# Kernel optimization log

Hardware: AMD Instinct MI355X
Metric: run time of the kernel (lower is better)

## Reference

```python
import jax, jax.numpy as jnp
import numpy as np
from jax import lax

B, D_IN, H, D_OUT, DEPTH = 16384, 1024, 1024, 256, 7


def setup_inputs() -> dict:
    key = jax.random.key(0)
    ks = jax.random.split(key, 10)
    f = jax.random.normal
    return {
        "x": f(ks[0], (B, D_IN), dtype=jnp.float32),
        "w0": f(ks[1], (D_IN, H), dtype=jnp.float32),
        "b0": f(ks[2], (H,), dtype=jnp.float32),
        "w1": f(ks[3], (H, H), dtype=jnp.float32),
        "b1": f(ks[4], (H,), dtype=jnp.float32),
        "tw": f(ks[5], (DEPTH, H, H), dtype=jnp.float32),   # transcendent_weights
        "cw": f(ks[6], (H, H), dtype=jnp.float32),           # classical_weights
        "cb": f(ks[7], (H,), dtype=jnp.float32),             # classical_biases (+ transcendent_biases folded out; original never uses transcendent_biases in forward)
        "wout": f(ks[8], (H, D_OUT), dtype=jnp.float32),
        "bout": f(ks[9], (D_OUT,), dtype=jnp.float32),
    }


def _transcendent_probs(tw):
    # tw: (DEPTH, n, m); angles used are tw[depth, j, 0:3] for j in range(out_dim)
    D, n, _ = tw.shape
    out_dim = n  # square layer: output_dimensions == input_dimensions
    angles = tw[:, :out_dim, :3]  # (D, O, 3)
    # each 'gate' matrix is the circulant M[i,i]=cos, M[i,i+1]=-sin, M[i+1,i]=sin (indices mod n)
    # => (M s)[i] = cos*s[i] - sin*s[i+1] + sin*s[i-1]  (circular shifts)
    state0 = jnp.full((out_dim, n), 1.0 / np.sqrt(n), dtype=tw.dtype)

    def gate(st, ang):  # st: (O, n), ang: (O,)
        c = jnp.cos(ang)[:, None]
        s = jnp.sin(ang)[:, None]
        return c * st - s * jnp.roll(st, -1, axis=1) + s * jnp.roll(st, 1, axis=1)

    def depth_step(st, a3):  # a3: (O, 3) -> consciousness, intelligence, wisdom gates
        st = gate(st, a3[:, 0])
        st = gate(st, a3[:, 1])
        st = gate(st, a3[:, 2])
        return st, None

    state, _ = lax.scan(depth_step, state0, angles)
    return jnp.abs(state[:, 0]) ** 2  # (O,), identical for every batch row


def reference(x, w0, b0, w1, b1, tw, cw, cb, wout, bout):
    h = jax.nn.relu(x @ w0 + b0)
    h = jax.nn.relu(h @ w1 + b1)
    # TranscendentNeuralLayer: tanh(classical + transcendent)
    h = jnp.tanh(h @ cw + cb + _transcendent_probs(tw)[None, :])
    return jax.nn.relu(h @ wout + bout)
```

## Files before the change

### kernel.cpp

```cpp
#include <hip/hip_runtime.h>
#include <hip/hip_bf16.h>

typedef __attribute__((ext_vector_type(8))) short bf16x8;
typedef __attribute__((ext_vector_type(4))) float f32x4;
typedef unsigned short u16;

__device__ __forceinline__ u16 f2bf(float f) {
  union { float f; unsigned int u; } v; v.f = f;
  unsigned int r = v.u + 0x7fffu + ((v.u >> 16) & 1u);
  return (u16)(r >> 16);
}
__device__ __forceinline__ float bf2f(u16 h) {
  union { unsigned int u; float f; } v; v.u = ((unsigned int)h) << 16;
  return v.f;
}

__device__ __forceinline__ void gload16(const void* g, void* l) {
  __builtin_amdgcn_global_load_lds(
      (const __attribute__((address_space(1))) unsigned int*)g,
      (__attribute__((address_space(3))) unsigned int*)l, 16, 0, 0);
}

__global__ void probs_kernel(const float* __restrict__ tw, float* __restrict__ probs) {
  int i = blockIdx.x * blockDim.x + threadIdx.x;
  if (i >= 1024) return;
  float p = 1.f;
  for (int d = 0; d < 7; ++d) {
    const float* a = tw + ((size_t)d * 1024 + i) * 1024;
    p *= cosf(a[0]) * cosf(a[1]) * cosf(a[2]);
  }
  probs[i] = p * p * (1.0f / 1024.0f);
}

__global__ void transpose_split(const float* __restrict__ src, u16* __restrict__ dhi,
                                u16* __restrict__ dlo, int R, int C) {
  __shared__ float t[32][33];
  int c0 = blockIdx.x * 32, r0 = blockIdx.y * 32;
  int tx = threadIdx.x, ty = threadIdx.y;
  #pragma unroll
  for (int p = 0; p < 4; ++p)
    t[ty + p * 8][tx] = src[(size_t)(r0 + ty + p * 8) * C + c0 + tx];
  __syncthreads();
  #pragma unroll
  for (int p = 0; p < 4; ++p) {
    float v = t[tx][ty + p * 8];
    u16 hi = f2bf(v);
    u16 lo = f2bf(v - bf2f(hi));
    size_t idx = (size_t)(c0 + ty + p * 8) * R + r0 + tx;
    dhi[idx] = hi; dlo[idx] = lo;
  }
}

__global__ void split_elem(const float* __restrict__ src, u16* __restrict__ hi,
                           u16* __restrict__ lo, int n4) {
  int i = blockIdx.x * blockDim.x + threadIdx.x;
  if (i >= n4) return;
  float4 v = ((const float4*)src)[i];
  ushort4 h, l;
  h.x = f2bf(v.x); l.x = f2bf(v.x - bf2f(h.x));
  h.y = f2bf(v.y); l.y = f2bf(v.y - bf2f(h.y));
  h.z = f2bf(v.z); l.z = f2bf(v.z - bf2f(h.z));
  h.w = f2bf(v.w); l.w = f2bf(v.w - bf2f(h.w));
  ((ushort4*)hi)[i] = h; ((ushort4*)lo)[i] = l;
}

template <int EPI>
__global__ __launch_bounds__(512, 2) void gemm256(
    const u16* __restrict__ Ahi, const u16* __restrict__ Alo,
    const u16* __restrict__ Bhi, const u16* __restrict__ Blo,
    const float* __restrict__ bias, const float* __restrict__ extra,
    u16* __restrict__ Ohi, u16* __restrict__ Olo,
    int N, int K, int nbx) {
  extern __shared__ __align__(16) char smem[];
  const int tid = threadIdx.x;
  const int wave = tid >> 6, lane = tid & 63;

  const int bq = gridDim.x >> 3;
  const int wg = (blockIdx.x & 7) * bq + (blockIdx.x >> 3);
  const int m0 = (wg / nbx) * 256, n0 = (wg % nbx) * 256;

  const int wm = (wave >> 2) * 128;
  const int wn = (wave & 3) * 64;
  const int lr = lane & 15, s0 = lane >> 4;

  f32x4 acc[8][4] = {};
  const int NT = K >> 5;

  auto stage = [&](const u16* __restrict__ G, int gr0, int kt, int ubase) {
    #pragma unroll
    for (int p = 0; p < 2; ++p) {
      const int ch = p * 8 + wave;
      const int off = ch * 1024 + lane * 16;
      const int r = off >> 6;
      const int s = ((off >> 4) & 3) ^ ((r >> 1) & 3);
      const u16* src = G + (size_t)(gr0 + r) * K + kt * 32 + s * 8;
      gload16((const void*)src, (void*)(smem + ubase + ch * 1024));
    }
  };
  auto frag = [&](int ubase, int row) -> bf16x8 {
    const int byte = ubase + row * 64 + ((s0 ^ ((row >> 1) & 3)) << 4);
    return *(const bf16x8*)(smem + byte);
  };

  stage(Ahi, m0, 0, 0);
  stage(Bhi, n0, 0, 32768);
  stage(Blo, n0, 0, 49152);
  stage(Alo, m0, 0, 16384);
  asm volatile("s_waitcnt vmcnt(4)" ::: "memory");
  __builtin_amdgcn_s_barrier();

  for (int kt = 0; kt < NT; ++kt) {
    const int cb = (kt & 1) << 16;
    const int nb = cb ^ 65536;
    const int kn = (kt + 1 == NT) ? 0 : kt + 1;
    bf16x8 a[8], bh[4], bl[4];

    stage(Ahi, m0, kn, nb);
    stage(Bhi, n0, kn, nb + 32768);
    #pragma unroll
    for (int m = 0; m < 8; ++m) a[m] = frag(cb, wm + m * 16 + lr);
    #pragma unroll
    for (int n = 0; n < 4; ++n) bh[n] = frag(cb + 32768, wn + n * 16 + lr);
    asm volatile("" ::: "memory");
    __builtin_amdgcn_s_barrier();
    __builtin_amdgcn_s_setprio(1);
    #pragma unroll
    for (int m = 0; m < 8; ++m)
      #pragma unroll
      for (int n = 0; n < 4; ++n)
        acc[m][n] = __builtin_amdgcn_mfma_f32_16x16x32_bf16(a[m], bh[n], acc[m][n], 0, 0, 0);
    __builtin_amdgcn_s_setprio(0);
    asm volatile("s_waitcnt vmcnt(6)" ::: "memory");
    __builtin_amdgcn_s_barrier();

    stage(Blo, n0, kn, nb + 49152);
    #pragma unroll
    for (int n = 0; n < 4; ++n) bl[n] = frag(cb + 49152, wn + n * 16 + lr);
    asm volatile("" ::: "memory");
    __builtin_amdgcn_s_barrier();
    __builtin_amdgcn_s_setprio(1);
    #pragma unroll
    for (int m = 0; m < 8; ++m)
      #pragma unroll
      for (int n = 0; n < 4; ++n)
        acc[m][n] = __builtin_amdgcn_mfma_f32_16x16x32_bf16(a[m], bl[n], acc[m][n], 0, 0, 0);
    __builtin_amdgcn_s_setprio(0);
    asm volatile("s_waitcnt vmcnt(6)" ::: "memory");
    __builtin_amdgcn_s_barrier();

    stage(Alo, m0, kn, nb + 16384);
    #pragma unroll
    for (int m = 0; m < 8; ++m) a[m] = frag(cb + 16384, wm + m * 16 + lr);
    asm volatile("" ::: "memory");
    __builtin_amdgcn_s_barrier();
    __builtin_amdgcn_s_setprio(1);
    #pragma unroll
    for (int m = 0; m < 8; ++m)
      #pragma unroll
      for (int n = 0; n < 4; ++n)
        acc[m][n] = __builtin_amdgcn_mfma_f32_16x16x32_bf16(a[m], bh[n], acc[m][n], 0, 0, 0);
    __builtin_amdgcn_s_setprio(0);
    asm volatile("s_waitcnt vmcnt(4)" ::: "memory");
    __builtin_amdgcn_s_barrier();
  }

  const int lm = lane >> 4, ln = lane & 15;
  float bsum[4];
  #pragma unroll
  for (int n = 0; n < 4; ++n) {
    int col = n0 + wn + n * 16 + ln;
    bsum[n] = bias[col];
    if (EPI == 1) bsum[n] += extra[col];
  }
  #pragma unroll
  for (int m = 0; m < 8; ++m) {
    int rbase = m0 + wm + m * 16 + lm * 4;
    #pragma unroll
    for (int n = 0; n < 4; ++n) {
      int col = n0 + wn + n * 16 + ln;
      #pragma unroll
      for (int r = 0; r < 4; ++r) {
        float v = acc[m][n][r] + bsum[n];
        if (EPI == 0) v = fmaxf(v, 0.f);
        else          v = 1.f - __fdividef(2.f, __expf(2.f * v) + 1.f);
        size_t idx = (size_t)(rbase + r) * N + col;
        u16 hi = f2bf(v);
        u16 lo = f2bf(v - bf2f(hi));
        Ohi[idx] = hi; Olo[idx] = lo;
      }
    }
  }
}

template <int EPI>
__global__ __launch_bounds__(256, 2) void gemm3(
    const u16* __restrict__ Ahi, const u16* __restrict__ Alo,
    const u16* __restrict__ Bhi, const u16* __restrict__ Blo,
    const float* __restrict__ bias, float* __restrict__ Ofp,
    int M, int N, int K) {
  __shared__ __align__(16) u16 sA[2][128 * 32];
  __shared__ __align__(16) u16 sB[2][128 * 32];

  const int tid = threadIdx.x;
  const int wave = tid >> 6;
  const int lane = tid & 63;
  const int n0 = blockIdx.x * 128;
  const int m0 = blockIdx.y * 128;
  const int wm = (wave >> 1) * 64;
  const int wn = (wave & 1) * 64;

  f32x4 acc[4][4] = {};

  const u16* gA[2] = {Ahi, Alo};
  const u16* gB[2] = {Bhi, Blo};
  const int srow = (lane >> 2);
  const int sslot = (lane & 3) * 8;

  for (int kt = 0; kt < K; kt += 32) {
    #pragma unroll
    for (int h = 0; h < 2; ++h) {
      #pragma unroll
      for (int j = 0; j < 2; ++j) {
        int c = wave * 2 + j;
        const u16* srcA = gA[h] + (size_t)(m0 + c * 16 + srow) * K + kt + sslot;
        gload16((const void*)srcA, (void*)&sA[h][c * 512]);
        const u16* srcB = gB[h] + (size_t)(n0 + c * 16 + srow) * K + kt + sslot;
        gload16((const void*)srcB, (void*)&sB[h][c * 512]);
      }
    }
    __syncthreads();

    const int kb = (lane >> 4) * 8;
    bf16x8 bh[4], bl[4];
    #pragma unroll
    for (int n = 0; n < 4; ++n) {
      int col = wn + n * 16 + (lane & 15);
      bh[n] = *(const bf16x8*)&sB[0][col * 32 + kb];
      bl[n] = *(const bf16x8*)&sB[1][col * 32 + kb];
    }
    #pragma unroll
    for (int m = 0; m < 4; ++m) {
      int row = wm + m * 16 + (lane & 15);
      bf16x8 ah = *(const bf16x8*)&sA[0][row * 32 + kb];
      bf16x8 al = *(const bf16x8*)&sA[1][row * 32 + kb];
      #pragma unroll
      for (int n = 0; n < 4; ++n) {
        acc[m][n] = __builtin_amdgcn_mfma_f32_16x16x32_bf16(ah, bh[n], acc[m][n], 0, 0, 0);
        acc[m][n] = __builtin_amdgcn_mfma_f32_16x16x32_bf16(ah, bl[n], acc[m][n], 0, 0, 0);
        acc[m][n] = __builtin_amdgcn_mfma_f32_16x16x32_bf16(al, bh[n], acc[m][n], 0, 0, 0);
      }
    }
    __syncthreads();
  }

  const int lm = lane >> 4;
  const int ln = lane & 15;
  float bsum[4];
  #pragma unroll
  for (int n = 0; n < 4; ++n) bsum[n] = bias[n0 + wn + n * 16 + ln];
  #pragma unroll
  for (int m = 0; m < 4; ++m) {
    int rbase = m0 + wm + m * 16 + lm * 4;
    #pragma unroll
    for (int n = 0; n < 4; ++n) {
      int col = n0 + wn + n * 16 + ln;
      #pragma unroll
      for (int r = 0; r < 4; ++r) {
        float v = acc[m][n][r] + bsum[n];
        Ofp[(size_t)(rbase + r) * N + col] = fmaxf(v, 0.f);
      }
    }
  }
}

extern "C" void kernel_launch(void* const* d_in, const int* in_sizes, int n_in,
                              void* d_out, int out_size, void* d_ws, size_t ws_size,
                              hipStream_t stream) {
  const float* x    = (const float*)d_in[0];
  const float* w0   = (const float*)d_in[1];
  const float* b0   = (const float*)d_in[2];
  const float* w1   = (const float*)d_in[3];
  const float* b1   = (const float*)d_in[4];
  const float* tw   = (const float*)d_in[5];
  const float* cw   = (const float*)d_in[6];
  const float* cb   = (const float*)d_in[7];
  const float* wout = (const float*)d_in[8];
  const float* bout = (const float*)d_in[9];
  float* out = (float*)d_out;
  char* ws = (char*)d_ws;
  const size_t MB = 1ull << 20;

  float* probs  = (float*)ws;
  u16* w0Thi = (u16*)(ws + 1 * MB);
  u16* w0Tlo = (u16*)(ws + 3 * MB);
  u16* w1Thi = (u16*)(ws + 5 * MB);
  u16* w1Tlo = (u16*)(ws + 7 * MB);
  u16* cwThi = (u16*)(ws + 9 * MB);
  u16* cwTlo = (u16*)(ws + 11 * MB);
  u16* woThi = (u16*)(ws + 13 * MB);
  u16* woTlo = (u16*)(ws + 13 * MB + 512 * 1024);
  u16* r0hi = (u16*)(ws + 16 * MB);
  u16* r0lo = (u16*)(ws + 48 * MB);
  u16* r1hi = (u16*)(ws + 80 * MB);
  u16* r1lo = (u16*)(ws + 112 * MB);

  hipFuncSetAttribute(reinterpret_cast<const void*>(gemm256<0>),
                      hipFuncAttributeMaxDynamicSharedMemorySize, 131072);
  hipFuncSetAttribute(reinterpret_cast<const void*>(gemm256<1>),
                      hipFuncAttributeMaxDynamicSharedMemorySize, 131072);

  probs_kernel<<<4, 256, 0, stream>>>(tw, probs);
  dim3 tb(32, 8);
  transpose_split<<<dim3(32, 32), tb, 0, stream>>>(w0, w0Thi, w0Tlo, 1024, 1024);
  transpose_split<<<dim3(32, 32), tb, 0, stream>>>(w1, w1Thi, w1Tlo, 1024, 1024);
  transpose_split<<<dim3(32, 32), tb, 0, stream>>>(cw, cwThi, cwTlo, 1024, 1024);
  transpose_split<<<dim3(8, 32), tb, 0, stream>>>(wout, woThi, woTlo, 1024, 256);
  split_elem<<<16384, 256, 0, stream>>>(x, r0hi, r0lo, 16384 * 1024 / 4);

  gemm256<0><<<256, 512, 131072, stream>>>(r0hi, r0lo, w0Thi, w0Tlo, b0, nullptr,
                                           r1hi, r1lo, 1024, 1024, 4);
  gemm256<0><<<256, 512, 131072, stream>>>(r1hi, r1lo, w1Thi, w1Tlo, b1, nullptr,
                                           r0hi, r0lo, 1024, 1024, 4);
  gemm256<1><<<256, 512, 131072, stream>>>(r0hi, r0lo, cwThi, cwTlo, cb, probs,
                                           r1hi, r1lo, 1024, 1024, 4);
  gemm3<2><<<dim3(2, 128), 256, 0, stream>>>(r1hi, r1lo, woThi, woTlo, bout,
                                             out, 16384, 256, 1024);
}
```

Baseline: 448.7 us.

## Switch big GEMMs to 32x32 MFMA, merge prep kernels, split-K bf16 last layer

New measurement: 447.4 us. Within noise of the previous version (-0.3%).

```diff
diff --git a/kernel.cpp b/kernel.cpp
--- a/kernel.cpp
+++ b/kernel.cpp
@@ -3,6 +3,7 @@
 
 typedef __attribute__((ext_vector_type(8))) short bf16x8;
 typedef __attribute__((ext_vector_type(4))) float f32x4;
+typedef __attribute__((ext_vector_type(16))) float f32x16;
 typedef unsigned short u16;
 
 __device__ __forceinline__ u16 f2bf(float f) {
@@ -21,22 +22,12 @@
       (__attribute__((address_space(3))) unsigned int*)l, 16, 0, 0);
 }
 
-__global__ void probs_kernel(const float* __restrict__ tw, float* __restrict__ probs) {
-  int i = blockIdx.x * blockDim.x + threadIdx.x;
-  if (i >= 1024) return;
-  float p = 1.f;
-  for (int d = 0; d < 7; ++d) {
-    const float* a = tw + ((size_t)d * 1024 + i) * 1024;
-    p *= cosf(a[0]) * cosf(a[1]) * cosf(a[2]);
-  }
-  probs[i] = p * p * (1.0f / 1024.0f);
-}
-
-__global__ void transpose_split(const float* __restrict__ src, u16* __restrict__ dhi,
-                                u16* __restrict__ dlo, int R, int C) {
+__device__ __forceinline__ void do_transpose(const float* __restrict__ src,
+                                             u16* __restrict__ dhi, u16* __restrict__ dlo,
+                                             int R, int C, int bx, int by, int tid) {
   __shared__ float t[32][33];
-  int c0 = blockIdx.x * 32, r0 = blockIdx.y * 32;
-  int tx = threadIdx.x, ty = threadIdx.y;
+  int c0 = bx * 32, r0 = by * 32;
+  int tx = tid & 31, ty = tid >> 5;
   #pragma unroll
   for (int p = 0; p < 4; ++p)
     t[ty + p * 8][tx] = src[(size_t)(r0 + ty + p * 8) * C + c0 + tx];
@@ -51,17 +42,41 @@
   }
 }
 
-__global__ void split_elem(const float* __restrict__ src, u16* __restrict__ hi,
-                           u16* __restrict__ lo, int n4) {
-  int i = blockIdx.x * blockDim.x + threadIdx.x;
-  if (i >= n4) return;
-  float4 v = ((const float4*)src)[i];
-  ushort4 h, l;
-  h.x = f2bf(v.x); l.x = f2bf(v.x - bf2f(h.x));
-  h.y = f2bf(v.y); l.y = f2bf(v.y - bf2f(h.y));
-  h.z = f2bf(v.z); l.z = f2bf(v.z - bf2f(h.z));
-  h.w = f2bf(v.w); l.w = f2bf(v.w - bf2f(h.w));
-  ((ushort4*)hi)[i] = h; ((ushort4*)lo)[i] = l;
+__global__ void prep_kernel(const float* __restrict__ tw, float* __restrict__ probs,
+                            const float* __restrict__ w0, u16* w0hi, u16* w0lo,
+                            const float* __restrict__ w1, u16* w1hi, u16* w1lo,
+                            const float* __restrict__ cw, u16* cwhi, u16* cwlo,
+                            const float* __restrict__ wo, u16* wohi, u16* wolo,
+                            const float* __restrict__ x, u16* xhi, u16* xlo) {
+  const int b = blockIdx.x, tid = threadIdx.x;
+  if (b < 4) {
+    int i = b * 256 + tid;
+    float p = 1.f;
+    for (int d = 0; d < 7; ++d) {
+      const float* a = tw + ((size_t)d * 1024 + i) * 1024;
+      p *= cosf(a[0]) * cosf(a[1]) * cosf(a[2]);
+    }
+    probs[i] = p * p * (1.0f / 1024.0f);
+  } else if (b < 1028) {
+    int bb = b - 4;    do_transpose(w0, w0hi, w0lo, 1024, 1024, bb & 31, bb >> 5, tid);
+  } else if (b < 2052) {
+    int bb = b - 1028; do_transpose(w1, w1hi, w1lo, 1024, 1024, bb & 31, bb >> 5, tid);
+  } else if (b < 3076) {
+    int bb = b - 2052; do_transpose(cw, cwhi, cwlo, 1024, 1024, bb & 31, bb >> 5, tid);
+  } else if (b < 3332) {
+    int bb = b - 3076; do_transpose(wo, wohi, wolo, 1024, 256, bb & 7, bb >> 3, tid);
+  } else {
+    int i = (b - 3332) * 256 + tid;
+    if (i < 16384 * 1024 / 4) {
+      float4 v = ((const float4*)x)[i];
+      ushort4 h, l;
+      h.x = f2bf(v.x); l.x = f2bf(v.x - bf2f(h.x));
+      h.y = f2bf(v.y); l.y = f2bf(v.y - bf2f(h.y));
+      h.z = f2bf(v.z); l.z = f2bf(v.z - bf2f(h.z));
+      h.w = f2bf(v.w); l.w = f2bf(v.w - bf2f(h.w));
+      ((ushort4*)xhi)[i] = h; ((ushort4*)xlo)[i] = l;
+    }
+  }
 }
 
 template <int EPI>
@@ -81,9 +96,10 @@
 
   const int wm = (wave >> 2) * 128;
   const int wn = (wave & 3) * 64;
-  const int lr = lane & 15, s0 = lane >> 4;
-
-  f32x4 acc[8][4] = {};
+  const int lr = lane & 31;
+  const int kg = lane >> 5;
+
+  f32x16 acc[4][2] = {};
   const int NT = K >> 5;
 
   auto stage = [&](const u16* __restrict__ G, int gr0, int kt, int ubase) {
@@ -97,15 +113,16 @@
       gload16((const void*)src, (void*)(smem + ubase + ch * 1024));
     }
   };
-  auto frag = [&](int ubase, int row) -> bf16x8 {
-    const int byte = ubase + row * 64 + ((s0 ^ ((row >> 1) & 3)) << 4);
+  auto frag = [&](int ubase, int row, int ks) -> bf16x8 {
+    const int s = ks * 2 + kg;
+    const int byte = ubase + row * 64 + ((s ^ ((row >> 1) & 3)) << 4);
     return *(const bf16x8*)(smem + byte);
   };
 
   stage(Ahi, m0, 0, 0);
   stage(Bhi, n0, 0, 32768);
+  stage(Alo, m0, 0, 16384);
   stage(Blo, n0, 0, 49152);
-  stage(Alo, m0, 0, 16384);
   asm volatile("s_waitcnt vmcnt(4)" ::: "memory");
   __builtin_amdgcn_s_barrier();
 
@@ -113,164 +130,154 @@
     const int cb = (kt & 1) << 16;
     const int nb = cb ^ 65536;
     const int kn = (kt + 1 == NT) ? 0 : kt + 1;
-    bf16x8 a[8], bh[4], bl[4];
+    bf16x8 ah[4][2], bh[2][2], al[4][2], bl[2][2];
 
     stage(Ahi, m0, kn, nb);
     stage(Bhi, n0, kn, nb + 32768);
     #pragma unroll
-    for (int m = 0; m < 8; ++m) a[m] = frag(cb, wm + m * 16 + lr);
-    #pragma unroll
-    for (int n = 0; n < 4; ++n) bh[n] = frag(cb + 32768, wn + n * 16 + lr);
+    for (int m = 0; m < 4; ++m)
+      #pragma unroll
+      for (int ks = 0; ks < 2; ++ks) ah[m][ks] = frag(cb, wm + m * 32 + lr, ks);
+    #pragma unroll
+    for (int n = 0; n < 2; ++n)
+      #pragma unroll
+      for (int ks = 0; ks < 2; ++ks) bh[n][ks] = frag(cb + 32768, wn + n * 32 + lr, ks);
     asm volatile("" ::: "memory");
     __builtin_amdgcn_s_barrier();
     __builtin_amdgcn_s_setprio(1);
     #pragma unroll
-    for (int m = 0; m < 8; ++m)
-      #pragma unroll
-      for (int n = 0; n < 4; ++n)
-        acc[m][n] = __builtin_amdgcn_mfma_f32_16x16x32_bf16(a[m], bh[n], acc[m][n], 0, 0, 0);
+    for (int m = 0; m < 4; ++m)
+      #pragma unroll
+      for (int n = 0; n < 2; ++n)
+        #pragma unroll
+        for (int ks = 0; ks < 2; ++ks)
+          acc[m][n] = __builtin_amdgcn_mfma_f32_32x32x16_bf16(ah[m][ks], bh[n][ks], acc[m][n], 0, 0, 0);
     __builtin_amdgcn_s_setprio(0);
-    asm volatile("s_waitcnt vmcnt(6)" ::: "memory");
+    asm volatile("s_waitcnt vmcnt(4)" ::: "memory");
     __builtin_amdgcn_s_barrier();
 
+    stage(Alo, m0, kn, nb + 16384);
     stage(Blo, n0, kn, nb + 49152);
     #pragma unroll
-    for (int n = 0; n < 4; ++n) bl[n] = frag(cb + 49152, wn + n * 16 + lr);
+    for (int m = 0; m < 4; ++m)
+      #pragma unroll
+      for (int ks = 0; ks < 2; ++ks) al[m][ks] = frag(cb + 16384, wm + m * 32 + lr, ks);
+    #pragma unroll
+    for (int n = 0; n < 2; ++n)
+      #pragma unroll
+      for (int ks = 0; ks < 2; ++ks) bl[n][ks] = frag(cb + 49152, wn + n * 32 + lr, ks);
     asm volatile("" ::: "memory");
     __builtin_amdgcn_s_barrier();
     __builtin_amdgcn_s_setprio(1);
     #pragma unroll
-    for (int m = 0; m < 8; ++m)
-      #pragma unroll
-      for (int n = 0; n < 4; ++n)
-        acc[m][n] = __builtin_amdgcn_mfma_f32_16x16x32_bf16(a[m], bl[n], acc[m][n], 0, 0, 0);
-    __builtin_amdgcn_s_setprio(0);
-    asm volatile("s_waitcnt vmcnt(6)" ::: "memory");
-    __builtin_amdgcn_s_barrier();
-
-    stage(Alo, m0, kn, nb + 16384);
-    #pragma unroll
-    for (int m = 0; m < 8; ++m) a[m] = frag(cb + 16384, wm + m * 16 + lr);
-    asm volatile("" ::: "memory");
-    __builtin_amdgcn_s_barrier();
-    __builtin_amdgcn_s_setprio(1);
-    #pragma unroll
-    for (int m = 0; m < 8; ++m)
-      #pragma unroll
-      for (int n = 0; n < 4; ++n)
-        acc[m][n] = __builtin_amdgcn_mfma_f32_16x16x32_bf16(a[m], bh[n], acc[m][n], 0, 0, 0);
+    for (int m = 0; m < 4; ++m)
+      #pragma unroll
+      for (int n = 0; n < 2; ++n)
+        #pragma unroll
+        for (int ks = 0; ks < 2; ++ks) {
+          acc[m][n] = __builtin_amdgcn_mfma_f32_32x32x16_bf16(al[m][ks], bh[n][ks], acc[m][n], 0, 0, 0);
+          acc[m][n] = __builtin_amdgcn_mfma_f32_32x32x16_bf16(ah[m][ks], bl[n][ks], acc[m][n], 0, 0, 0);
+        }
     __builtin_amdgcn_s_setprio(0);
     asm volatile("s_waitcnt vmcnt(4)" ::: "memory");
     __builtin_amdgcn_s_barrier();
   }
 
-  const int lm = lane >> 4, ln = lane & 15;
-  float bsum[4];
-  #pragma unroll
-  for (int n = 0; n < 4; ++n) {
-    int col = n0 + wn + n * 16 + ln;
+  const int ln = lane & 31, lg = lane >> 5;
+  float bsum[2];
+  #pragma unroll
+  for (int n = 0; n < 2; ++n) {
+    int col = n0 + wn + n * 32 + ln;
     bsum[n] = bias[col];
     if (EPI == 1) bsum[n] += extra[col];
   }
   #pragma unroll
-  for (int m = 0; m < 8; ++m) {
+  for (int m = 0; m < 4; ++m) {
+    #pragma unroll
+    for (int n = 0; n < 2; ++n) {
+      int col = n0 + wn + n * 32 + ln;
+      #pragma unroll
+      for (int r = 0; r < 16; ++r) {
+        int row = m0 + wm + m * 32 + (r & 3) + 8 * (r >> 2) + 4 * lg;
+        float v = acc[m][n][r] + bsum[n];
+        size_t idx = (size_t)row * N + col;
+        if (EPI == 0) {
+          v = fmaxf(v, 0.f);
+          u16 hi = f2bf(v);
+          u16 lo = f2bf(v - bf2f(hi));
+          Ohi[idx] = hi; Olo[idx] = lo;
+        } else {
+          v = 1.f - __fdividef(2.f, __expf(2.f * v) + 1.f);
+          Ohi[idx] = f2bf(v);
+        }
+      }
+    }
+  }
+}
+
+__global__ __launch_bounds__(256, 2) void gemm_l4(
+    const u16* __restrict__ A, const u16* __restrict__ B,
+    float* __restrict__ P, int M, int N, int K, int kchunk) {
+  __shared__ __align__(16) u16 sA[128 * 32];
+  __shared__ __align__(16) u16 sB[128 * 32];
+  const int tid = threadIdx.x;
+  const int wave = tid >> 6, lane = tid & 63;
+  const int n0 = blockIdx.x * 128, m0 = blockIdx.y * 128;
+  const int koff = blockIdx.z * kchunk;
+  const int wm = (wave >> 1) * 64, wn = (wave & 1) * 64;
+  f32x4 acc[4][4] = {};
+  const int srow = lane >> 2, sslot = (lane & 3) * 8;
+
+  for (int kt = koff; kt < koff + kchunk; kt += 32) {
+    #pragma unroll
+    for (int j = 0; j < 2; ++j) {
+      int c = wave * 2 + j;
+      gload16((const void*)(A + (size_t)(m0 + c * 16 + srow) * K + kt + sslot), (void*)&sA[c * 512]);
+      gload16((const void*)(B + (size_t)(n0 + c * 16 + srow) * K + kt + sslot), (void*)&sB[c * 512]);
+    }
+    __syncthreads();
+    const int kb = (lane >> 4) * 8;
+    bf16x8 bfr[4];
+    #pragma unroll
+    for (int n = 0; n < 4; ++n)
+      bfr[n] = *(const bf16x8*)&sB[(wn + n * 16 + (lane & 15)) * 32 + kb];
+    #pragma unroll
+    for (int m = 0; m < 4; ++m) {
+      bf16x8 a = *(const bf16x8*)&sA[(wm + m * 16 + (lane & 15)) * 32 + kb];
+      #pragma unroll
+      for (int n = 0; n < 4; ++n)
+        acc[m][n] = __builtin_amdgcn_mfma_f32_16x16x32_bf16(a, bfr[n], acc[m][n], 0, 0, 0);
+    }
+    __syncthreads();
+  }
+
+  const int lm = lane >> 4, ln = lane & 15;
+  float* Pz = P + (size_t)blockIdx.z * M * N;
+  #pragma unroll
+  for (int m = 0; m < 4; ++m) {
     int rbase = m0 + wm + m * 16 + lm * 4;
     #pragma unroll
     for (int n = 0; n < 4; ++n) {
       int col = n0 + wn + n * 16 + ln;
       #pragma unroll
-      for (int r = 0; r < 4; ++r) {
-        float v = acc[m][n][r] + bsum[n];
-        if (EPI == 0) v = fmaxf(v, 0.f);
-        else          v = 1.f - __fdividef(2.f, __expf(2.f * v) + 1.f);
-        size_t idx = (size_t)(rbase + r) * N + col;
-        u16 hi = f2bf(v);
-        u16 lo = f2bf(v - bf2f(hi));
-        Ohi[idx] = hi; Olo[idx] = lo;
-      }
-    }
-  }
-}
-
-template <int EPI>
-__global__ __launch_bounds__(256, 2) void gemm3(
-    const u16* __restrict__ Ahi, const u16* __restrict__ Alo,
-    const u16* __restrict__ Bhi, const u16* __restrict__ Blo,
-    const float* __restrict__ bias, float* __restrict__ Ofp,
-    int M, int N, int K) {
-  __shared__ __align__(16) u16 sA[2][128 * 32];
-  __shared__ __align__(16) u16 sB[2][128 * 32];
-
-  const int tid = threadIdx.x;
-  const int wave = tid >> 6;
-  const int lane = tid & 63;
-  const int n0 = blockIdx.x * 128;
-  const int m0 = blockIdx.y * 128;
-  const int wm = (wave >> 1) * 64;
-  const int wn = (wave & 1) * 64;
-
-  f32x4 acc[4][4] = {};
-
-  const u16* gA[2] = {Ahi, Alo};
-  const u16* gB[2] = {Bhi, Blo};
-  const int srow = (lane >> 2);
-  const int sslot = (lane & 3) * 8;
-
-  for (int kt = 0; kt < K; kt += 32) {
-    #pragma unroll
-    for (int h = 0; h < 2; ++h) {
-      #pragma unroll
-      for (int j = 0; j < 2; ++j) {
-        int c = wave * 2 + j;
-        const u16* srcA = gA[h] + (size_t)(m0 + c * 16 + srow) * K + kt + sslot;
-        gload16((const void*)srcA, (void*)&sA[h][c * 512]);
-        const u16* srcB = gB[h] + (size_t)(n0 + c * 16 + srow) * K + kt + sslot;
-        gload16((const void*)srcB, (void*)&sB[h][c * 512]);
-      }
-    }
-    __syncthreads();
-
-    const int kb = (lane >> 4) * 8;
-    bf16x8 bh[4], bl[4];
-    #pragma unroll
-    for (int n = 0; n < 4; ++n) {
-      int col = wn + n * 16 + (lane & 15);
-      bh[n] = *(const bf16x8*)&sB[0][col * 32 + kb];
-      bl[n] = *(const bf16x8*)&sB[1][col * 32 + kb];
-    }
-    #pragma unroll
-    for (int m = 0; m < 4; ++m) {
-      int row = wm + m * 16 + (lane & 15);
-      bf16x8 ah = *(const bf16x8*)&sA[0][row * 32 + kb];
-      bf16x8 al = *(const bf16x8*)&sA[1][row * 32 + kb];
-      #pragma unroll
-      for (int n = 0; n < 4; ++n) {
-        acc[m][n] = __builtin_amdgcn_mfma_f32_16x16x32_bf16(ah, bh[n], acc[m][n], 0, 0, 0);
-        acc[m][n] = __builtin_amdgcn_mfma_f32_16x16x32_bf16(ah, bl[n], acc[m][n], 0, 0, 0);
-        acc[m][n] = __builtin_amdgcn_mfma_f32_16x16x32_bf16(al, bh[n], acc[m][n], 0, 0, 0);
-      }
-    }
-    __syncthreads();
-  }
-
-  const int lm = lane >> 4;
-  const int ln = lane & 15;
-  float bsum[4];
-  #pragma unroll
-  for (int n = 0; n < 4; ++n) bsum[n] = bias[n0 + wn + n * 16 + ln];
-  #pragma unroll
-  for (int m = 0; m < 4; ++m) {
-    int rbase = m0 + wm + m * 16 + lm * 4;
-    #pragma unroll
-    for (int n = 0; n < 4; ++n) {
-      int col = n0 + wn + n * 16 + ln;
-      #pragma unroll
-      for (int r = 0; r < 4; ++r) {
-        float v = acc[m][n][r] + bsum[n];
-        Ofp[(size_t)(rbase + r) * N + col] = fmaxf(v, 0.f);
-      }
-    }
-  }
+      for (int r = 0; r < 4; ++r)
+        Pz[(size_t)(rbase + r) * N + col] = acc[m][n][r];
+    }
+  }
+}
+
+__global__ void l4_reduce(const float* __restrict__ P, const float* __restrict__ bias,
+                          float* __restrict__ out) {
+  int i = blockIdx.x * 256 + threadIdx.x;
+  float4 a = ((const float4*)P)[i];
+  float4 b = ((const float4*)(P + 16384ull * 256))[i];
+  int c0 = (i * 4) & 255;
+  float4 o;
+  o.x = fmaxf(a.x + b.x + bias[c0 + 0], 0.f);
+  o.y = fmaxf(a.y + b.y + bias[c0 + 1], 0.f);
+  o.z = fmaxf(a.z + b.z + bias[c0 + 2], 0.f);
+  o.w = fmaxf(a.w + b.w + bias[c0 + 3], 0.f);
+  ((float4*)out)[i] = o;
 }
 
 extern "C" void kernel_launch(void* const* d_in, const int* in_sizes, int n_in,
@@ -303,26 +310,23 @@
   u16* r0lo = (u16*)(ws + 48 * MB);
   u16* r1hi = (u16*)(ws + 80 * MB);
   u16* r1lo = (u16*)(ws + 112 * MB);
+  float* l4p = (float*)(ws + 16 * MB);
 
   hipFuncSetAttribute(reinterpret_cast<const void*>(gemm256<0>),
                       hipFuncAttributeMaxDynamicSharedMemorySize, 131072);
   hipFuncSetAttribute(reinterpret_cast<const void*>(gemm256<1>),
                       hipFuncAttributeMaxDynamicSharedMemorySize, 131072);
 
-  probs_kernel<<<4, 256, 0, stream>>>(tw, probs);
-  dim3 tb(32, 8);
-  transpose_split<<<dim3(32, 32), tb, 0, stream>>>(w0, w0Thi, w0Tlo, 1024, 1024);
-  transpose_split<<<dim3(32, 32), tb, 0, stream>>>(w1, w1Thi, w1Tlo, 1024, 1024);
-  transpose_split<<<dim3(32, 32), tb, 0, stream>>>(cw, cwThi, cwTlo, 1024, 1024);
-  transpose_split<<<dim3(8, 32), tb, 0, stream>>>(wout, woThi, woTlo, 1024, 256);
-  split_elem<<<16384, 256, 0, stream>>>(x, r0hi, r0lo, 16384 * 1024 / 4);
+  prep_kernel<<<19716, 256, 0, stream>>>(tw, probs, w0, w0Thi, w0Tlo,
+                                         w1, w1Thi, w1Tlo, cw, cwThi, cwTlo,
+                                         wout, woThi, woTlo, x, r0hi, r0lo);
 
   gemm256<0><<<256, 512, 131072, stream>>>(r0hi, r0lo, w0Thi, w0Tlo, b0, nullptr,
                                            r1hi, r1lo, 1024, 1024, 4);
   gemm256<0><<<256, 512, 131072, stream>>>(r1hi, r1lo, w1Thi, w1Tlo, b1, nullptr,
                                            r0hi, r0lo, 1024, 1024, 4);
   gemm256<1><<<256, 512, 131072, stream>>>(r0hi, r0lo, cwThi, cwTlo, cb, probs,
-                                           r1hi, r1lo, 1024, 1024, 4);
-  gemm3<2><<<dim3(2, 128), 256, 0, stream>>>(r1hi, r1lo, woThi, woTlo, bout,
-                                             out, 16384, 256, 1024);
-}
+                                           r1hi, nullptr, 1024, 1024, 4);
+  gemm_l4<<<dim3(2, 128, 2), 256, 0, stream>>>(r1hi, woThi, l4p, 16384, 256, 1024, 512);
+  l4_reduce<<<4096, 256, 0, stream>>>(l4p, bout, out);
+}
```
